# Optimization experiments

Hardware: AMD Instinct MI355X
Metric: run time of the kernel (lower is better)

Reference implementation:

```python
import jax, jax.numpy as jnp
import numpy as np
import math

N_HEAD = 12


def setup_inputs() -> dict:
    key = jax.random.key(0)
    k1, k2, k3 = jax.random.split(key, 3)
    B, T, C = 4, 2048, 768
    x = jax.random.normal(k1, (B, T, C), dtype=jnp.float32)
    W = jax.random.normal(k2, (C, 3 * C), dtype=jnp.float32) * 0.02
    b = jax.random.normal(k3, (3 * C,), dtype=jnp.float32) * 0.02
    return {"x": x, "W": W, "b": b}


def reference(x, W, b):
    B, T, C = x.shape
    H = N_HEAD
    d = C // H
    qkv = x @ W + b                                # [B,T,3C]
    q, k, v = jnp.split(qkv, 3, axis=-1)           # each [B,T,C]
    q = q.reshape(B, T, H, d).transpose(0, 2, 1, 3)  # [B,H,T,d]
    k = k.reshape(B, T, H, d).transpose(0, 2, 1, 3)
    v = v.reshape(B, T, H, d).transpose(0, 2, 1, 3)
    # NOTE: source multiplies by sqrt(d) (not divides) -- faithful reproduction.
    att = jnp.einsum('bhqd,bhkd->bhqk', q, k) * (1.0 * math.sqrt(d))
    causal = jnp.tril(jnp.ones((T, T), dtype=bool))  # [T,T]
    att = jnp.where(causal[None, None, :, :], att, -jnp.inf)
    att = jax.nn.softmax(att, axis=-1)
    y = jnp.einsum('bhqk,bhkd->bhqd', att, v)      # [B,H,T,d]
    y = y.transpose(0, 2, 1, 3).reshape(B, T, C)   # [B,T,C]
    return y
```

## Files before the change

kernel.cpp:

```cpp
#include <hip/hip_runtime.h>
#include <math.h>

#define B_ 4
#define T_ 2048
#define C_ 768
#define H_ 12
#define D_ 64
#define N3C (3*C_)
#define BH_ (B_*H_)
#define QSCALE 11.5415603f

typedef float f32x4 __attribute__((ext_vector_type(4)));
typedef _Float16 f16x8 __attribute__((ext_vector_type(8)));
typedef unsigned short ushort_t;

__device__ __forceinline__ void async16(const void* g, void* l) {
    __builtin_amdgcn_global_load_lds(
        (const __attribute__((address_space(1))) unsigned int*)(g),
        (__attribute__((address_space(3))) unsigned int*)(l),
        16, 0, 0);
}

__device__ __forceinline__ unsigned pk_f16(float a, float b) {
    __fp16 r2[2];
    *(__fp16 __attribute__((ext_vector_type(2)))*)r2 = __builtin_amdgcn_cvt_pkrtz(a, b);
    return *(unsigned*)r2;
}

__global__ __launch_bounds__(256) void conv_xw(const float* __restrict__ x,
                                               const float* __restrict__ W,
                                               _Float16* __restrict__ Xh,
                                               _Float16* __restrict__ Wh)
{
    __shared__ float tile[64][65];
    int bid = blockIdx.x;
    int tid = threadIdx.x;
    if (bid < 3072) {
        int idx = bid * 256 + tid;
        const float4 a = *reinterpret_cast<const float4*>(&x[(size_t)idx * 8]);
        const float4 b = *reinterpret_cast<const float4*>(&x[(size_t)idx * 8 + 4]);
        f16x8 o = {(_Float16)a.x, (_Float16)a.y, (_Float16)a.z, (_Float16)a.w,
                   (_Float16)b.x, (_Float16)b.y, (_Float16)b.z, (_Float16)b.w};
        *reinterpret_cast<f16x8*>(&Xh[(size_t)idx * 8]) = o;
    } else {
        int b2 = bid - 3072;
        int n0 = (b2 % 36) * 64, k0 = (b2 / 36) * 64;
        #pragma unroll
        for (int t = 0; t < 16; ++t) {
            int c = t * 256 + tid;
            int kr = c >> 6, nc = c & 63;
            tile[kr][nc] = W[(size_t)(k0 + kr) * N3C + n0 + nc];
        }
        __syncthreads();
        #pragma unroll
        for (int t = 0; t < 16; ++t) {
            int c = t * 256 + tid;
            int nr = c >> 6, kc = c & 63;
            Wh[(size_t)(n0 + nr) * C_ + k0 + kc] = (_Float16)tile[kc][nr];
        }
    }
}

__global__ __launch_bounds__(256) void qkv_gemm(const _Float16* __restrict__ Xh,
                                                const _Float16* __restrict__ Wh,
                                                const float* __restrict__ bias,
                                                _Float16* __restrict__ Qf,
                                                _Float16* __restrict__ Kf,
                                                _Float16* __restrict__ Vt)
{
    __shared__ __align__(16) ushort_t SMEM[128 * 64 * 2];
    ushort_t* As = SMEM;
    ushort_t* Bs = SMEM + 128 * 64;

    int tid = threadIdx.x, lane = tid & 63, w = tid >> 6;
    int wm = w >> 1, wn = w & 1;
    int l15 = lane & 15, l4 = lane >> 4;
    int srow = lane >> 3;
    int scol = (((lane & 7) ^ srow)) << 3;

    int wg = blockIdx.x;
    int l = (wg & 7) * 144 + (wg >> 3);
    int mt = l / 18, nt = l % 18;
    int row0 = mt * 128, col0 = nt * 128;

    f32x4 acc[4][4];
    #pragma unroll
    for (int i = 0; i < 4; ++i)
        #pragma unroll
        for (int j = 0; j < 4; ++j)
            acc[i][j] = f32x4{0.f, 0.f, 0.f, 0.f};

    const char* AsC = (const char*)As;
    const char* BsC = (const char*)Bs;

    for (int k0 = 0; k0 < C_; k0 += 64) {
        __syncthreads();
        #pragma unroll
        for (int j = 0; j < 4; ++j) {
            int rowb = w * 32 + j * 8;
            async16(Xh + (size_t)(row0 + rowb + srow) * C_ + k0 + scol, &As[rowb * 64]);
            async16(Wh + (size_t)(col0 + rowb + srow) * C_ + k0 + scol, &Bs[rowb * 64]);
        }
        __syncthreads();

        #pragma unroll
        for (int kk = 0; kk < 2; ++kk) {
            f16x8 af[4], bfr[4];
            #pragma unroll
            for (int m = 0; m < 4; ++m) {
                int r = wm * 64 + m * 16 + l15;
                af[m] = *reinterpret_cast<const f16x8*>(AsC + r * 128 + ((kk * 64 + l4 * 16) ^ ((r & 7) << 4)));
            }
            #pragma unroll
            for (int n = 0; n < 4; ++n) {
                int r = wn * 64 + n * 16 + l15;
                bfr[n] = *reinterpret_cast<const f16x8*>(BsC + r * 128 + ((kk * 64 + l4 * 16) ^ ((r & 7) << 4)));
            }
            #pragma unroll
            for (int m = 0; m < 4; ++m)
                #pragma unroll
                for (int n = 0; n < 4; ++n)
                    acc[m][n] = __builtin_amdgcn_mfma_f32_16x16x32_f16(af[m], bfr[n], acc[m][n], 0, 0, 0);
        }
    }

    __syncthreads();
    char* EB = (char*)SMEM;
    int p = col0 / C_;

    if (p < 2) {
        #pragma unroll
        for (int n = 0; n < 4; ++n) {
            int col = wn * 64 + n * 16 + l15;
            float bv = bias[col0 + col];
            #pragma unroll
            for (int m = 0; m < 4; ++m) {
                #pragma unroll
                for (int r = 0; r < 4; ++r) {
                    int row = wm * 64 + m * 16 + l4 * 4 + r;
                    float v = acc[m][n][r] + bv;
                    if (p == 0) v *= QSCALE;
                    int off = row * 256 + ((col * 2) ^ ((row & 7) << 4));
                    *reinterpret_cast<_Float16*>(EB + off) = (_Float16)v;
                }
            }
        }
        __syncthreads();
        int ti = tid >> 1, half = tid & 1;
        int grow = row0 + ti;
        int bq = grow >> 11, t = grow & (T_ - 1);
        int rem = (col0 + half * 64) - p * C_;
        int hh = rem >> 6;
        _Float16* dst = (p == 0 ? Qf : Kf) + ((size_t)(bq * H_ + hh) * T_ + t) * D_;
        #pragma unroll
        for (int u = 0; u < 8; ++u) {
            int off = ti * 256 + ((half * 128 + u * 16) ^ ((ti & 7) << 4));
            *reinterpret_cast<uint4*>((char*)dst + u * 16) = *reinterpret_cast<const uint4*>(EB + off);
        }
    } else {
        #pragma unroll
        for (int n = 0; n < 4; ++n) {
            int col = wn * 64 + n * 16 + l15;
            float bv = bias[col0 + col];
            #pragma unroll
            for (int m = 0; m < 4; ++m) {
                int row = wm * 64 + m * 16 + l4 * 4;
                uint2 pk;
                pk.x = pk_f16(acc[m][n][0] + bv, acc[m][n][1] + bv);
                pk.y = pk_f16(acc[m][n][2] + bv, acc[m][n][3] + bv);
                int off = col * 256 + ((row * 2) ^ ((col & 15) << 4));
                *reinterpret_cast<uint2*>(EB + off) = pk;
            }
        }
        __syncthreads();
        int dcol = tid >> 1, half = tid & 1;
        int rem = (col0 + dcol) - 1536;
        int hh = rem >> 6, dd = rem & 63;
        int bq = row0 >> 11, t0 = row0 & (T_ - 1);
        _Float16* dst = Vt + ((size_t)(bq * H_ + hh) * D_ + dd) * T_ + t0 + half * 64;
        #pragma unroll
        for (int u = 0; u < 8; ++u) {
            int off = dcol * 256 + ((half * 128 + u * 16) ^ ((dcol & 15) << 4));
            *reinterpret_cast<uint4*>((char*)dst + u * 16) = *reinterpret_cast<const uint4*>(EB + off);
        }
    }
}

__device__ const unsigned char ITEM_QT[24] = {15,15,7,14,14,13,13,6,12,12,11,11,5,10,10,9,9,4,8,8,3,2,1,0};
__device__ const unsigned char ITEM_CH[24] = { 0, 1,0, 0, 1, 0, 1,0, 0, 1, 0, 1,0, 0, 1,0,1,0,0,1,0,0,0,0};

__global__ __launch_bounds__(256, 4) void attn(const _Float16* __restrict__ Qf,
                                               const _Float16* __restrict__ Kf,
                                               const _Float16* __restrict__ Vt,
                                               float* __restrict__ out,
                                               float* __restrict__ Op,
                                               float* __restrict__ ML)
{
    __shared__ __align__(16) char smem[40960];
    ushort_t* lds = (ushort_t*)smem;

    int tid = threadIdx.x, lane = tid & 63, w = tid >> 6;
    int l15 = lane & 15, l4 = lane >> 4;
    int bid = blockIdx.x;
    int rank = bid / BH_;
    int bh = bid % BH_;
    int qt = ITEM_QT[rank];
    int ch = ITEM_CH[rank];
    int b = bh / H_, h = bh % H_;
    int q0 = qt * 128;

    int it0 = (qt < 8 || ch == 0) ? 0 : (qt + 1);
    int it1 = (qt >= 8 && ch == 0) ? (qt + 1) : (2 * qt + 2);

    f16x8 qf[2][2];
    #pragma unroll
    for (int qs = 0; qs < 2; ++qs) {
        int q = q0 + w * 32 + qs * 16 + l15;
        const _Float16* ph = Qf + ((size_t)bh * T_ + q) * D_;
        qf[qs][0] = *reinterpret_cast<const f16x8*>(ph + l4 * 8);
        qf[qs][1] = *reinterpret_cast<const f16x8*>(ph + 32 + l4 * 8);
    }

    f32x4 yacc[2][4];
    #pragma unroll
    for (int qs = 0; qs < 2; ++qs)
        #pragma unroll
        for (int dt = 0; dt < 4; ++dt)
            yacc[qs][dt] = f32x4{0.f, 0.f, 0.f, 0.f};
    float m_run[2] = {-INFINITY, -INFINITY};
    float l_run[2] = {0.f, 0.f};

    int srow = lane >> 3;
    int scol = ((lane & 7) ^ srow) << 3;
    char* PwB = (char*)(lds + 16384 + w * 1024);
    int pswz = (l15 & 7) << 4;

    const _Float16* kp[2];
    const _Float16* vp[2];
    #pragma unroll
    for (int j = 0; j < 2; ++j) {
        int row = (w * 2 + j) * 8 + srow;
        kp[j] = Kf + ((size_t)bh * T_ + it0 * 64 + row) * D_ + scol;
        vp[j] = Vt + ((size_t)bh * D_ + row) * T_ + it0 * 64 + scol;
    }

    #pragma unroll
    for (int j = 0; j < 2; ++j) {
        ushort_t* dK = lds + (w * 2 + j) * 512;
        async16(kp[j], dK);
        async16(vp[j], dK + 4096);
        kp[j] += 64 * D_;
        vp[j] += 64;
    }
    __syncthreads();

    int cur = 0;
    for (int it = it0; it < it1; ++it) {
        int k0 = it * 64;
        int nxt = cur ^ 1;
        if (it + 1 < it1) {
            #pragma unroll
            for (int j = 0; j < 2; ++j) {
                ushort_t* dK = lds + nxt * 8192 + (w * 2 + j) * 512;
                async16(kp[j], dK);
                async16(vp[j], dK + 4096);
                kp[j] += 64 * D_;
                vp[j] += 64;
            }
        }

        if (k0 <= q0 + w * 32 + 31) {
            const char* KHc = (const char*)(lds + cur * 8192);
            const char* VSc = KHc + 8192;
            f16x8 pa[2][2];
            f32x4 sa[2][4];
            #pragma unroll
            for (int qs = 0; qs < 2; ++qs)
                #pragma unroll
                for (int i = 0; i < 4; ++i) sa[qs][i] = f32x4{0.f, 0.f, 0.f, 0.f};

            __builtin_amdgcn_s_setprio(1);
            #pragma unroll
            for (int kt = 0; kt < 4; ++kt) {
                int krow = kt * 16 + l15;
                int swz = (krow & 7) << 4;
                #pragma unroll
                for (int dh = 0; dh < 2; ++dh) {
                    f16x8 kf = *reinterpret_cast<const f16x8*>(KHc + krow * 128 + ((dh * 64 + l4 * 16) ^ swz));
                    sa[0][kt] = __builtin_amdgcn_mfma_f32_16x16x32_f16(kf, qf[0][dh], sa[0][kt], 0, 0, 0);
                    sa[1][kt] = __builtin_amdgcn_mfma_f32_16x16x32_f16(kf, qf[1][dh], sa[1][kt], 0, 0, 0);
                }
            }
            __builtin_amdgcn_s_setprio(0);

            #pragma unroll
            for (int qs = 0; qs < 2; ++qs) {
                if (it >= 2 * qt) {
                    int qg = q0 + w * 32 + qs * 16 + l15;
                    #pragma unroll
                    for (int kt = 0; kt < 4; ++kt)
                        #pragma unroll
                        for (int r = 0; r < 4; ++r)
                            if (k0 + kt * 16 + l4 * 4 + r > qg) sa[qs][kt][r] = -INFINITY;
                }

                float mx = sa[qs][0][0];
                #pragma unroll
                for (int kt = 0; kt < 4; ++kt)
                    #pragma unroll
                    for (int r = 0; r < 4; ++r) mx = fmaxf(mx, sa[qs][kt][r]);
                mx = fmaxf(mx, __shfl_xor(mx, 16));
                mx = fmaxf(mx, __shfl_xor(mx, 32));

                float mn;
                if (__all(mx <= m_run[qs] + 8.0f)) {
                    mn = m_run[qs];
                } else {
                    mn = fmaxf(m_run[qs], mx);
                    float sc = exp2f(m_run[qs] - mn);
                    m_run[qs] = mn;
                    l_run[qs] *= sc;
                    #pragma unroll
                    for (int dt = 0; dt < 4; ++dt) yacc[qs][dt] *= sc;
                }

                float p[4][4];
                float rs = 0.f;
                #pragma unroll
                for (int kt = 0; kt < 4; ++kt)
                    #pragma unroll
                    for (int r = 0; r < 4; ++r) {
                        p[kt][r] = exp2f(sa[qs][kt][r] - mn);
                        rs += p[kt][r];
                    }
                l_run[qs] += rs;

                #pragma unroll
                for (int kt = 0; kt < 4; ++kt) {
                    uint2 pw;
                    pw.x = pk_f16(p[kt][0], p[kt][1]);
                    pw.y = pk_f16(p[kt][2], p[kt][3]);
                    int off = (l15 * 128 + kt * 32 + l4 * 8) ^ pswz;
                    *reinterpret_cast<uint2*>(PwB + off) = pw;
                }
                pa[qs][0] = *reinterpret_cast<const f16x8*>(PwB + ((l15 * 128 + l4 * 16) ^ pswz));
                pa[qs][1] = *reinterpret_cast<const f16x8*>(PwB + ((l15 * 128 + 64 + l4 * 16) ^ pswz));
            }

            __builtin_amdgcn_s_setprio(1);
            #pragma unroll
            for (int dt = 0; dt < 4; ++dt) {
                int vrow = dt * 16 + l15;
                int vswz = (vrow & 7) << 4;
                #pragma unroll
                for (int kk = 0; kk < 2; ++kk) {
                    f16x8 vf = *reinterpret_cast<const f16x8*>(VSc + vrow * 128 + ((kk * 64 + l4 * 16) ^ vswz));
                    yacc[0][dt] = __builtin_amdgcn_mfma_f32_16x16x32_f16(vf, pa[0][kk], yacc[0][dt], 0, 0, 0);
                    yacc[1][dt] = __builtin_amdgcn_mfma_f32_16x16x32_f16(vf, pa[1][kk], yacc[1][dt], 0, 0, 0);
                }
            }
            __builtin_amdgcn_s_setprio(0);
        }
        __syncthreads();
        cur = nxt;
    }

    #pragma unroll
    for (int qs = 0; qs < 2; ++qs) {
        l_run[qs] += __shfl_xor(l_run[qs], 16);
        l_run[qs] += __shfl_xor(l_run[qs], 32);
    }

    float* ot = (float*)smem;
    if (qt < 8) {
        #pragma unroll
        for (int qs = 0; qs < 2; ++qs) {
            float inv = 1.0f / l_run[qs];
            int rq = w * 32 + qs * 16 + l15;
            #pragma unroll
            for (int dt = 0; dt < 4; ++dt)
                #pragma unroll
                for (int r = 0; r < 4; ++r)
                    ot[rq * 68 + dt * 16 + l4 * 4 + r] = yacc[qs][dt][r] * inv;
        }
        __syncthreads();
        int rr = tid >> 1, c0 = (tid & 1) * 32;
        size_t ob = ((size_t)(b * T_ + q0 + rr)) * C_ + h * D_ + c0;
        #pragma unroll
        for (int u = 0; u < 8; ++u) {
            float4 v = *reinterpret_cast<const float4*>(&ot[rr * 68 + c0 + u * 4]);
            *reinterpret_cast<float4*>(&out[ob + u * 4]) = v;
        }
    } else {
        #pragma unroll
        for (int qs = 0; qs < 2; ++qs) {
            int rq = w * 32 + qs * 16 + l15;
            #pragma unroll
            for (int dt = 0; dt < 4; ++dt)
                #pragma unroll
                for (int r = 0; r < 4; ++r)
                    ot[rq * 68 + dt * 16 + l4 * 4 + r] = yacc[qs][dt][r];
        }
        if (l4 == 0) {
            float* mlp = ML + (((size_t)bh * 8 + (qt - 8)) * 2 + ch) * 256;
            #pragma unroll
            for (int qs = 0; qs < 2; ++qs) {
                int ql = w * 32 + qs * 16 + l15;
                mlp[ql] = m_run[qs];
                mlp[128 + ql] = l_run[qs];
            }
        }
        __syncthreads();
        int rr = tid >> 1, c0 = (tid & 1) * 32;
        float* dst = Op + (((size_t)bh * 8 + (qt - 8)) * 2 + ch) * 8192 + rr * 64 + c0;
        #pragma unroll
        for (int u = 0; u < 8; ++u) {
            float4 v = *reinterpret_cast<const float4*>(&ot[rr * 68 + c0 + u * 4]);
            *reinterpret_cast<float4*>(&dst[u * 4]) = v;
        }
    }
}

__global__ __launch_bounds__(256) void merge(const float* __restrict__ Op,
                                             const float* __restrict__ ML,
                                             float* __restrict__ out)
{
    int gid = blockIdx.x * 256 + threadIdx.x;
    int row = gid >> 4, seg = gid & 15;
    int q = row & 127, qt8 = (row >> 7) & 7, bh = row >> 10;

    size_t mbase = ((size_t)bh * 8 + qt8) * 2 * 256;
    float m1 = ML[mbase + q],       l1 = ML[mbase + 128 + q];
    float m2 = ML[mbase + 256 + q], l2 = ML[mbase + 256 + 128 + q];
    float m = fmaxf(m1, m2);
    float a1 = exp2f(m1 - m), a2 = exp2f(m2 - m);
    float inv = 1.0f / (l1 * a1 + l2 * a2);

    size_t obase = ((size_t)bh * 8 + qt8) * 2 * 8192 + q * 64 + seg * 4;
    float4 o1 = *reinterpret_cast<const float4*>(&Op[obase]);
    float4 o2 = *reinterpret_cast<const float4*>(&Op[obase + 8192]);
    float4 r;
    r.x = (o1.x * a1 + o2.x * a2) * inv;
    r.y = (o1.y * a1 + o2.y * a2) * inv;
    r.z = (o1.z * a1 + o2.z * a2) * inv;
    r.w = (o1.w * a1 + o2.w * a2) * inv;

    int b = bh / H_, h = bh % H_;
    int t = (qt8 + 8) * 128 + q;
    *reinterpret_cast<float4*>(&out[((size_t)(b * T_ + t)) * C_ + h * D_ + seg * 4]) = r;
}

extern "C" void kernel_launch(void* const* d_in, const int* in_sizes, int n_in,
                              void* d_out, int out_size, void* d_ws, size_t ws_size,
                              hipStream_t stream)
{
    const float* x    = (const float*)d_in[0];
    const float* W    = (const float*)d_in[1];
    const float* bias = (const float*)d_in[2];

    const size_t per = (size_t)BH_ * T_ * D_;
    _Float16* Qf = (_Float16*)d_ws;
    _Float16* Kf = Qf + per;
    _Float16* Vt = Kf + per;
    _Float16* Xh = Vt + per;
    _Float16* Wh = Xh + (size_t)8192 * C_;
    float*    Op = (float*)(Wh + (size_t)N3C * C_);
    float*    ML = Op + (size_t)48 * 8 * 2 * 8192;

    conv_xw<<<dim3(3072 + 432), 256, 0, stream>>>(x, W, Xh, Wh);
    qkv_gemm<<<dim3(64 * 18), 256, 0, stream>>>(Xh, Wh, bias, Qf, Kf, Vt);
    attn<<<dim3(24 * BH_), 256, 0, stream>>>(Qf, Kf, Vt, (float*)d_out, Op, ML);
    merge<<<dim3(49152 * 16 / 256), 256, 0, stream>>>(Op, ML, (float*)d_out);
}
```

Measured before the change: 134.8 us.

## Double attention query tile to 256 rows with 8-wave blocks

Each attention block now handles 256 query rows using 512 threads (8 waves), so every K/V tile loaded into LDS serves twice as many queries. The work list, the split/merge scheme and the epilogue are rescaled to match: the output staging runs in two passes, and the causal mask check is now decided per wave. This halves K/V global traffic per query. The cost is fewer, larger blocks, more LDS per block, coarser load balance across the causal triangle, and idle waves on the diagonal tiles.

```diff
diff --git a/kernel.cpp b/kernel.cpp
--- a/kernel.cpp
+++ b/kernel.cpp
@@ -186,17 +186,17 @@
     }
 }
 
-__device__ const unsigned char ITEM_QT[24] = {15,15,7,14,14,13,13,6,12,12,11,11,5,10,10,9,9,4,8,8,3,2,1,0};
-__device__ const unsigned char ITEM_CH[24] = { 0, 1,0, 0, 1, 0, 1,0, 0, 1, 0, 1,0, 0, 1,0,1,0,0,1,0,0,0,0};
-
-__global__ __launch_bounds__(256, 4) void attn(const _Float16* __restrict__ Qf,
+__device__ const unsigned char ITEM_QT[12] = {7,7,3,6,6,5,5,2,4,4,1,0};
+__device__ const unsigned char ITEM_CH[12] = {0,1,0,0,1,0,1,0,0,1,0,0};
+
+__global__ __launch_bounds__(512, 6) void attn(const _Float16* __restrict__ Qf,
                                                const _Float16* __restrict__ Kf,
                                                const _Float16* __restrict__ Vt,
                                                float* __restrict__ out,
                                                float* __restrict__ Op,
                                                float* __restrict__ ML)
 {
-    __shared__ __align__(16) char smem[40960];
+    __shared__ __align__(16) char smem[49152];
     ushort_t* lds = (ushort_t*)smem;
 
     int tid = threadIdx.x, lane = tid & 63, w = tid >> 6;
@@ -207,10 +207,10 @@
     int qt = ITEM_QT[rank];
     int ch = ITEM_CH[rank];
     int b = bh / H_, h = bh % H_;
-    int q0 = qt * 128;
-
-    int it0 = (qt < 8 || ch == 0) ? 0 : (qt + 1);
-    int it1 = (qt >= 8 && ch == 0) ? (qt + 1) : (2 * qt + 2);
+    int q0 = qt * 256;
+
+    int it0 = (qt < 4 || ch == 0) ? 0 : 2 * (qt + 1);
+    int it1 = (qt >= 4 && ch == 0) ? 2 * (qt + 1) : 4 * (qt + 1);
 
     f16x8 qf[2][2];
     #pragma unroll
@@ -235,22 +235,16 @@
     char* PwB = (char*)(lds + 16384 + w * 1024);
     int pswz = (l15 & 7) << 4;
 
-    const _Float16* kp[2];
-    const _Float16* vp[2];
-    #pragma unroll
-    for (int j = 0; j < 2; ++j) {
-        int row = (w * 2 + j) * 8 + srow;
-        kp[j] = Kf + ((size_t)bh * T_ + it0 * 64 + row) * D_ + scol;
-        vp[j] = Vt + ((size_t)bh * D_ + row) * T_ + it0 * 64 + scol;
-    }
-
-    #pragma unroll
-    for (int j = 0; j < 2; ++j) {
-        ushort_t* dK = lds + (w * 2 + j) * 512;
-        async16(kp[j], dK);
-        async16(vp[j], dK + 4096);
-        kp[j] += 64 * D_;
-        vp[j] += 64;
+    int prow = w * 8 + srow;
+    const _Float16* kp = Kf + ((size_t)bh * T_ + it0 * 64 + prow) * D_ + scol;
+    const _Float16* vp = Vt + ((size_t)bh * D_ + prow) * T_ + it0 * 64 + scol;
+
+    {
+        ushort_t* dK = lds + w * 512;
+        async16(kp, dK);
+        async16(vp, dK + 4096);
+        kp += 64 * D_;
+        vp += 64;
     }
     __syncthreads();
 
@@ -259,14 +253,11 @@
         int k0 = it * 64;
         int nxt = cur ^ 1;
         if (it + 1 < it1) {
-            #pragma unroll
-            for (int j = 0; j < 2; ++j) {
-                ushort_t* dK = lds + nxt * 8192 + (w * 2 + j) * 512;
-                async16(kp[j], dK);
-                async16(vp[j], dK + 4096);
-                kp[j] += 64 * D_;
-                vp[j] += 64;
-            }
+            ushort_t* dK = lds + nxt * 8192 + w * 512;
+            async16(kp, dK);
+            async16(vp, dK + 4096);
+            kp += 64 * D_;
+            vp += 64;
         }
 
         if (k0 <= q0 + w * 32 + 31) {
@@ -293,9 +284,10 @@
             }
             __builtin_amdgcn_s_setprio(0);
 
+            bool diag = (k0 + 63 > q0 + w * 32);
             #pragma unroll
             for (int qs = 0; qs < 2; ++qs) {
-                if (it >= 2 * qt) {
+                if (diag) {
                     int qg = q0 + w * 32 + qs * 16 + l15;
                     #pragma unroll
                     for (int kt = 0; kt < 4; ++kt)
@@ -371,52 +363,52 @@
         l_run[qs] += __shfl_xor(l_run[qs], 32);
     }
 
+    bool split = (qt >= 4);
+    int item = split ? ((bh * 4 + (qt - 4)) * 2 + ch) : 0;
+
+    if (split && l4 == 0) {
+        float* mlp = ML + (size_t)item * 512;
+        #pragma unroll
+        for (int qs = 0; qs < 2; ++qs) {
+            int ql = w * 32 + qs * 16 + l15;
+            mlp[ql] = m_run[qs];
+            mlp[256 + ql] = l_run[qs];
+        }
+    }
+
     float* ot = (float*)smem;
-    if (qt < 8) {
-        #pragma unroll
-        for (int qs = 0; qs < 2; ++qs) {
-            float inv = 1.0f / l_run[qs];
-            int rq = w * 32 + qs * 16 + l15;
-            #pragma unroll
-            for (int dt = 0; dt < 4; ++dt)
-                #pragma unroll
-                for (int r = 0; r < 4; ++r)
-                    ot[rq * 68 + dt * 16 + l4 * 4 + r] = yacc[qs][dt][r] * inv;
-        }
-        __syncthreads();
-        int rr = tid >> 1, c0 = (tid & 1) * 32;
-        size_t ob = ((size_t)(b * T_ + q0 + rr)) * C_ + h * D_ + c0;
-        #pragma unroll
-        for (int u = 0; u < 8; ++u) {
-            float4 v = *reinterpret_cast<const float4*>(&ot[rr * 68 + c0 + u * 4]);
-            *reinterpret_cast<float4*>(&out[ob + u * 4]) = v;
-        }
-    } else {
-        #pragma unroll
-        for (int qs = 0; qs < 2; ++qs) {
-            int rq = w * 32 + qs * 16 + l15;
-            #pragma unroll
-            for (int dt = 0; dt < 4; ++dt)
-                #pragma unroll
-                for (int r = 0; r < 4; ++r)
-                    ot[rq * 68 + dt * 16 + l4 * 4 + r] = yacc[qs][dt][r];
-        }
-        if (l4 == 0) {
-            float* mlp = ML + (((size_t)bh * 8 + (qt - 8)) * 2 + ch) * 256;
+    #pragma unroll
+    for (int pass = 0; pass < 2; ++pass) {
+        __syncthreads();
+        if ((w >> 2) == pass) {
+            int wl = w & 3;
             #pragma unroll
             for (int qs = 0; qs < 2; ++qs) {
-                int ql = w * 32 + qs * 16 + l15;
-                mlp[ql] = m_run[qs];
-                mlp[128 + ql] = l_run[qs];
-            }
-        }
-        __syncthreads();
-        int rr = tid >> 1, c0 = (tid & 1) * 32;
-        float* dst = Op + (((size_t)bh * 8 + (qt - 8)) * 2 + ch) * 8192 + rr * 64 + c0;
-        #pragma unroll
-        for (int u = 0; u < 8; ++u) {
-            float4 v = *reinterpret_cast<const float4*>(&ot[rr * 68 + c0 + u * 4]);
-            *reinterpret_cast<float4*>(&dst[u * 4]) = v;
+                float inv = split ? 1.0f : (1.0f / l_run[qs]);
+                int rq = wl * 32 + qs * 16 + l15;
+                #pragma unroll
+                for (int dt = 0; dt < 4; ++dt)
+                    #pragma unroll
+                    for (int r = 0; r < 4; ++r)
+                        ot[rq * 68 + dt * 16 + l4 * 4 + r] = yacc[qs][dt][r] * inv;
+            }
+        }
+        __syncthreads();
+        int rr = tid >> 2, c0 = (tid & 3) * 16;
+        if (!split) {
+            size_t ob = ((size_t)(b * T_ + q0 + pass * 128 + rr)) * C_ + h * D_ + c0;
+            #pragma unroll
+            for (int u = 0; u < 4; ++u) {
+                float4 v = *reinterpret_cast<const float4*>(&ot[rr * 68 + c0 + u * 4]);
+                *reinterpret_cast<float4*>(&out[ob + u * 4]) = v;
+            }
+        } else {
+            float* dst = Op + (size_t)item * 16384 + (pass * 128 + rr) * 64 + c0;
+            #pragma unroll
+            for (int u = 0; u < 4; ++u) {
+                float4 v = *reinterpret_cast<const float4*>(&ot[rr * 68 + c0 + u * 4]);
+                *reinterpret_cast<float4*>(&dst[u * 4]) = v;
+            }
         }
     }
 }
@@ -427,18 +419,18 @@
 {
     int gid = blockIdx.x * 256 + threadIdx.x;
     int row = gid >> 4, seg = gid & 15;
-    int q = row & 127, qt8 = (row >> 7) & 7, bh = row >> 10;
-
-    size_t mbase = ((size_t)bh * 8 + qt8) * 2 * 256;
-    float m1 = ML[mbase + q],       l1 = ML[mbase + 128 + q];
-    float m2 = ML[mbase + 256 + q], l2 = ML[mbase + 256 + 128 + q];
+    int q = row & 255, qt4 = (row >> 8) & 3, bh = row >> 10;
+
+    size_t mbase = (size_t)(bh * 4 + qt4) * 2 * 512;
+    float m1 = ML[mbase + q],       l1 = ML[mbase + 256 + q];
+    float m2 = ML[mbase + 512 + q], l2 = ML[mbase + 512 + 256 + q];
     float m = fmaxf(m1, m2);
     float a1 = exp2f(m1 - m), a2 = exp2f(m2 - m);
     float inv = 1.0f / (l1 * a1 + l2 * a2);
 
-    size_t obase = ((size_t)bh * 8 + qt8) * 2 * 8192 + q * 64 + seg * 4;
+    size_t obase = (size_t)(bh * 4 + qt4) * 2 * 16384 + q * 64 + seg * 4;
     float4 o1 = *reinterpret_cast<const float4*>(&Op[obase]);
-    float4 o2 = *reinterpret_cast<const float4*>(&Op[obase + 8192]);
+    float4 o2 = *reinterpret_cast<const float4*>(&Op[obase + 16384]);
     float4 r;
     r.x = (o1.x * a1 + o2.x * a2) * inv;
     r.y = (o1.y * a1 + o2.y * a2) * inv;
@@ -446,7 +438,7 @@
     r.w = (o1.w * a1 + o2.w * a2) * inv;
 
     int b = bh / H_, h = bh % H_;
-    int t = (qt8 + 8) * 128 + q;
+    int t = (qt4 + 4) * 256 + q;
     *reinterpret_cast<float4*>(&out[((size_t)(b * T_ + t)) * C_ + h * D_ + seg * 4]) = r;
 }
 
@@ -465,10 +457,10 @@
     _Float16* Xh = Vt + per;
     _Float16* Wh = Xh + (size_t)8192 * C_;
     float*    Op = (float*)(Wh + (size_t)N3C * C_);
-    float*    ML = Op + (size_t)48 * 8 * 2 * 8192;
+    float*    ML = Op + (size_t)48 * 4 * 2 * 16384;
 
     conv_xw<<<dim3(3072 + 432), 256, 0, stream>>>(x, W, Xh, Wh);
     qkv_gemm<<<dim3(64 * 18), 256, 0, stream>>>(Xh, Wh, bias, Qf, Kf, Vt);
-    attn<<<dim3(24 * BH_), 256, 0, stream>>>(Qf, Kf, Vt, (float*)d_out, Op, ML);
+    attn<<<dim3(12 * BH_), 512, 0, stream>>>(Qf, Kf, Vt, (float*)d_out, Op, ML);
     merge<<<dim3(49152 * 16 / 256), 256, 0, stream>>>(Op, ML, (float*)d_out);
 }
```

New measurement: 351.0 us. 2.6x slower.

## Double-buffer QKV GEMM LDS tiles and overlap async loads with MFMA

Applied to the files above, without the earlier changes.

Moves the QKV projection GEMM from a single LDS buffer with two barriers per k-step to a double-buffered scheme. The next k-tile is prefetched with global_load_lds in two halves, each interleaved with half of the MFMA work, and only one barrier is used per iteration. This is meant to hide global-to-LDS latency behind compute. The cost is LDS use doubling to 64KB per block, which may reduce occupancy, plus more registers for the held B fragments.

```diff
diff --git a/kernel.cpp b/kernel.cpp
--- a/kernel.cpp
+++ b/kernel.cpp
@@ -68,9 +68,7 @@
                                                 _Float16* __restrict__ Kf,
                                                 _Float16* __restrict__ Vt)
 {
-    __shared__ __align__(16) ushort_t SMEM[128 * 64 * 2];
-    ushort_t* As = SMEM;
-    ushort_t* Bs = SMEM + 128 * 64;
+    __shared__ __align__(16) ushort_t SMEM[2 * 2 * 128 * 64];
 
     int tid = threadIdx.x, lane = tid & 63, w = tid >> 6;
     int wm = w >> 1, wn = w & 1;
@@ -90,41 +88,88 @@
         for (int j = 0; j < 4; ++j)
             acc[i][j] = f32x4{0.f, 0.f, 0.f, 0.f};
 
-    const char* AsC = (const char*)As;
-    const char* BsC = (const char*)Bs;
-
-    for (int k0 = 0; k0 < C_; k0 += 64) {
-        __syncthreads();
-        #pragma unroll
-        for (int j = 0; j < 4; ++j) {
-            int rowb = w * 32 + j * 8;
-            async16(Xh + (size_t)(row0 + rowb + srow) * C_ + k0 + scol, &As[rowb * 64]);
-            async16(Wh + (size_t)(col0 + rowb + srow) * C_ + k0 + scol, &Bs[rowb * 64]);
-        }
-        __syncthreads();
-
-        #pragma unroll
-        for (int kk = 0; kk < 2; ++kk) {
-            f16x8 af[4], bfr[4];
-            #pragma unroll
-            for (int m = 0; m < 4; ++m) {
+    #pragma unroll
+    for (int j = 0; j < 4; ++j) {
+        int rowb = w * 32 + j * 8;
+        async16(Xh + (size_t)(row0 + rowb + srow) * C_ + scol, &SMEM[rowb * 64]);
+        async16(Wh + (size_t)(col0 + rowb + srow) * C_ + scol, &SMEM[8192 + rowb * 64]);
+    }
+    __syncthreads();
+
+    int cur = 0;
+    for (int it = 0; it < 12; ++it) {
+        int nxt = cur ^ 1;
+        int k0n = (it + 1) * 64;
+        bool pf = (it + 1 < 12);
+        const char* AsC = (const char*)(SMEM + cur * 16384);
+        const char* BsC = AsC + 16384;
+        ushort_t* An = SMEM + nxt * 16384;
+        ushort_t* Bn = An + 8192;
+
+        if (pf) {
+            #pragma unroll
+            for (int j = 0; j < 2; ++j) {
+                int rowb = w * 32 + j * 8;
+                async16(Xh + (size_t)(row0 + rowb + srow) * C_ + k0n + scol, &An[rowb * 64]);
+                async16(Wh + (size_t)(col0 + rowb + srow) * C_ + k0n + scol, &Bn[rowb * 64]);
+            }
+        }
+        f16x8 bfr[4][2];
+        #pragma unroll
+        for (int n = 0; n < 4; ++n) {
+            int r = wn * 64 + n * 16 + l15;
+            #pragma unroll
+            for (int kk = 0; kk < 2; ++kk)
+                bfr[n][kk] = *reinterpret_cast<const f16x8*>(BsC + r * 128 + ((kk * 64 + l4 * 16) ^ ((r & 7) << 4)));
+        }
+        {
+            f16x8 af[2][2];
+            #pragma unroll
+            for (int m = 0; m < 2; ++m) {
                 int r = wm * 64 + m * 16 + l15;
-                af[m] = *reinterpret_cast<const f16x8*>(AsC + r * 128 + ((kk * 64 + l4 * 16) ^ ((r & 7) << 4)));
-            }
-            #pragma unroll
-            for (int n = 0; n < 4; ++n) {
-                int r = wn * 64 + n * 16 + l15;
-                bfr[n] = *reinterpret_cast<const f16x8*>(BsC + r * 128 + ((kk * 64 + l4 * 16) ^ ((r & 7) << 4)));
-            }
-            #pragma unroll
-            for (int m = 0; m < 4; ++m)
-                #pragma unroll
-                for (int n = 0; n < 4; ++n)
-                    acc[m][n] = __builtin_amdgcn_mfma_f32_16x16x32_f16(af[m], bfr[n], acc[m][n], 0, 0, 0);
-        }
-    }
-
-    __syncthreads();
+                #pragma unroll
+                for (int kk = 0; kk < 2; ++kk)
+                    af[m][kk] = *reinterpret_cast<const f16x8*>(AsC + r * 128 + ((kk * 64 + l4 * 16) ^ ((r & 7) << 4)));
+            }
+            #pragma unroll
+            for (int kk = 0; kk < 2; ++kk)
+                #pragma unroll
+                for (int m = 0; m < 2; ++m)
+                    #pragma unroll
+                    for (int n = 0; n < 4; ++n)
+                        acc[m][n] = __builtin_amdgcn_mfma_f32_16x16x32_f16(af[m][kk], bfr[n][kk], acc[m][n], 0, 0, 0);
+        }
+
+        if (pf) {
+            #pragma unroll
+            for (int j = 2; j < 4; ++j) {
+                int rowb = w * 32 + j * 8;
+                async16(Xh + (size_t)(row0 + rowb + srow) * C_ + k0n + scol, &An[rowb * 64]);
+                async16(Wh + (size_t)(col0 + rowb + srow) * C_ + k0n + scol, &Bn[rowb * 64]);
+            }
+        }
+        {
+            f16x8 af[2][2];
+            #pragma unroll
+            for (int m = 0; m < 2; ++m) {
+                int r = wm * 64 + (m + 2) * 16 + l15;
+                #pragma unroll
+                for (int kk = 0; kk < 2; ++kk)
+                    af[m][kk] = *reinterpret_cast<const f16x8*>(AsC + r * 128 + ((kk * 64 + l4 * 16) ^ ((r & 7) << 4)));
+            }
+            #pragma unroll
+            for (int kk = 0; kk < 2; ++kk)
+                #pragma unroll
+                for (int m = 0; m < 2; ++m)
+                    #pragma unroll
+                    for (int n = 0; n < 4; ++n)
+                        acc[m + 2][n] = __builtin_amdgcn_mfma_f32_16x16x32_f16(af[m][kk], bfr[n][kk], acc[m + 2][n], 0, 0, 0);
+        }
+
+        __syncthreads();
+        cur = nxt;
+    }
+
     char* EB = (char*)SMEM;
     int p = col0 / C_;
 
```

Result: faster. 130.5 us (-3.2%).
